# Kernel tuning notes

Hardware: AMD Instinct MI355X
Metric: run time of the kernel (lower is better)

The kernel has to match this reference:

```python
import jax, jax.numpy as jnp
import numpy as np

DIM = 1024
HEADS = 16
DIM_HEAD = 64
B = 4
N = 2048
INNER = HEADS * DIM_HEAD
SCALE = DIM_HEAD ** -0.5
NEG = -1e9


def setup_inputs() -> dict:
    key = jax.random.key(0)
    k1, k2, k3 = jax.random.split(key, 3)
    x = jax.random.normal(k1, (B, N, DIM), dtype=jnp.float32)
    w_qkv = jax.random.normal(k2, (DIM, 3 * INNER), dtype=jnp.float32) * (DIM ** -0.5)
    w_out = jax.random.normal(k3, (INNER, DIM), dtype=jnp.float32) * (INNER ** -0.5)
    b_out = jnp.zeros((DIM,), dtype=jnp.float32)
    return {"x": x, "w_qkv": w_qkv, "w_out": w_out, "b_out": b_out}


def reference(x, w_qkv, w_out, b_out):
    b, n, _ = x.shape
    qkv = x @ w_qkv  # [b, n, 3*inner]
    q, k, v = jnp.split(qkv, 3, axis=-1)
    # [b, n, inner] -> [b, h, n, d]
    split_heads = lambda t: t.reshape(b, n, HEADS, DIM_HEAD).transpose(0, 2, 1, 3)
    q, k, v = split_heads(q), split_heads(k), split_heads(v)
    dots = jnp.einsum('bhid,bhjd->bhij', q, k) * SCALE
    causal = jnp.tril(jnp.ones((n, n), dtype=bool))  # mask[i,j]=1 for j<=i
    dots = jnp.where(causal, dots, NEG)
    attn = jax.nn.softmax(dots, axis=-1)
    out = jnp.einsum('bhij,bhjd->bhid', attn, v)
    out = out.transpose(0, 2, 1, 3).reshape(b, n, INNER)
    return out @ w_out + b_out
```

## Files before the change

kernel.cpp:

```cpp
#include <hip/hip_runtime.h>

typedef unsigned short u16;
typedef __attribute__((ext_vector_type(8))) short short8;
typedef __attribute__((ext_vector_type(4))) float f32x4;
typedef __attribute__((ext_vector_type(4))) short short4v;

#define MFMA_BF16(a, b, c) __builtin_amdgcn_mfma_f32_16x16x32_bf16((a), (b), (c), 0, 0, 0)

__device__ __forceinline__ void gl2lds16(const u16* g, u16* l) {
  __builtin_amdgcn_global_load_lds(
      (const __attribute__((address_space(1))) unsigned int*)g,
      (__attribute__((address_space(3))) unsigned int*)l, 16, 0, 0);
}

__device__ __forceinline__ u16 f2bf(float f) {
  union { float f; unsigned u; } v; v.f = f;
  unsigned r = v.u + 0x7fffu + ((v.u >> 16) & 1u);
  return (u16)(r >> 16);
}

__global__ void fill_one_f32(float* p, int n) {
  int i = blockIdx.x * blockDim.x + threadIdx.x;
  if (i < n) p[i] = 1.0f;
}

__global__ void prep_k(const float* __restrict__ x, u16* __restrict__ Xb,
                       const float* __restrict__ w_qkv, u16* __restrict__ wqkvT,
                       const float* __restrict__ w_out, u16* __restrict__ woutT) {
  __shared__ float tile[32][33];
  const int bid = blockIdx.x, t = threadIdx.x;
  if (bid < 2048) {
    const int base = (bid * 256 + t) * 16;
#pragma unroll
    for (int h = 0; h < 2; ++h) {
      const f32x4 v0 = *(const f32x4*)&x[base + h * 8];
      const f32x4 v1 = *(const f32x4*)&x[base + h * 8 + 4];
      short8 o;
      o[0] = (short)f2bf(v0.x); o[1] = (short)f2bf(v0.y);
      o[2] = (short)f2bf(v0.z); o[3] = (short)f2bf(v0.w);
      o[4] = (short)f2bf(v1.x); o[5] = (short)f2bf(v1.y);
      o[6] = (short)f2bf(v1.z); o[7] = (short)f2bf(v1.w);
      *(short8*)&Xb[base + h * 8] = o;
    }
    return;
  }
  const float* src; u16* dst; int R, C, bx, by;
  if (bid < 5120) {
    const int tb = bid - 2048;
    src = w_qkv; dst = wqkvT; R = 1024; C = 3072; bx = tb % 96; by = tb / 96;
  } else {
    const int tb = bid - 5120;
    src = w_out; dst = woutT; R = 1024; C = 1024; bx = tb % 32; by = tb / 32;
  }
  const int tx = t & 31, ty = t >> 5;
  const int r0 = by * 32, c0 = bx * 32;
#pragma unroll
  for (int i = 0; i < 4; ++i)
    tile[ty + i * 8][tx] = src[(size_t)(r0 + ty + i * 8) * C + c0 + tx];
  __syncthreads();
#pragma unroll
  for (int i = 0; i < 4; ++i)
    dst[(size_t)(c0 + ty + i * 8) * R + r0 + tx] = f2bf(tile[tx][ty + i * 8]);
}

template <int MODE>
__launch_bounds__(256, 2)
__global__ void gemm_bt_k(const u16* __restrict__ A, const u16* __restrict__ Bt,
                          int K, int Ncols,
                          u16* __restrict__ O0, u16* __restrict__ O1,
                          u16* __restrict__ O2,
                          float* __restrict__ Of, const float* __restrict__ biasf) {
  __shared__ __align__(16) u16 Alds[128 * 32];
  __shared__ __align__(16) u16 Blds[128 * 32];
  const int t = threadIdx.x;
  const int w = t >> 6, l = t & 63;
  const int quad = l >> 4, l16 = l & 15;
  const int m0 = blockIdx.y * 128, n0 = blockIdx.x * 128;
  const int wm = w & 1, wn = w >> 1;

  f32x4 acc[4][4];
#pragma unroll
  for (int a = 0; a < 4; ++a)
#pragma unroll
    for (int b = 0; b < 4; ++b) acc[a][b] = (f32x4){0.f, 0.f, 0.f, 0.f};

  const int c0 = w * 128 + l;

#pragma unroll 1
  for (int k0 = 0; k0 < K; k0 += 32) {
    {
      int c = c0;
      gl2lds16(A + (size_t)(m0 + (c >> 2)) * K + k0 + (c & 3) * 8,
               (u16*)((char*)Alds + c * 16));
      gl2lds16(Bt + (size_t)(n0 + (c >> 2)) * K + k0 + (c & 3) * 8,
               (u16*)((char*)Blds + c * 16));
      c = c0 + 64;
      gl2lds16(A + (size_t)(m0 + (c >> 2)) * K + k0 + (c & 3) * 8,
               (u16*)((char*)Alds + c * 16));
      gl2lds16(Bt + (size_t)(n0 + (c >> 2)) * K + k0 + (c & 3) * 8,
               (u16*)((char*)Blds + c * 16));
    }
    __syncthreads();
    short8 av[4], bv[4];
#pragma unroll
    for (int a = 0; a < 4; ++a)
      av[a] = *(const short8*)&Alds[(wm * 64 + a * 16 + l16) * 32 + quad * 8];
#pragma unroll
    for (int b = 0; b < 4; ++b)
      bv[b] = *(const short8*)&Blds[(wn * 64 + b * 16 + l16) * 32 + quad * 8];
#pragma unroll
    for (int a = 0; a < 4; ++a)
#pragma unroll
      for (int b = 0; b < 4; ++b)
        acc[a][b] = MFMA_BF16(av[a], bv[b], acc[a][b]);
    __syncthreads();
  }

#pragma unroll
  for (int a = 0; a < 4; ++a)
#pragma unroll
    for (int b = 0; b < 4; ++b)
#pragma unroll
      for (int r = 0; r < 4; ++r) {
        const int row = m0 + wm * 64 + a * 16 + quad * 4 + r;
        const int col = n0 + wn * 64 + b * 16 + l16;
        const float v = acc[a][b][r];
        if (MODE == 0) {
          const int bb = row >> 11, n = row & 2047;
          const int which = col >> 10, j = col & 1023, h = j >> 6, d = j & 63;
          u16* dst = (which == 0) ? O0 : (which == 1) ? O1 : O2;
          dst[(((size_t)bb * 16 + h) * 2048 + n) * 64 + d] = f2bf(v);
        } else {
          Of[(size_t)row * Ncols + col] = v + biasf[col];
        }
      }
}

#define KS 72
__launch_bounds__(512, 4)
__global__ void flash_k4(const u16* __restrict__ Q, const u16* __restrict__ K,
                         const u16* __restrict__ V, u16* __restrict__ AO) {
  __shared__ __align__(16) u16 Klds[64 * KS];
  __shared__ __align__(16) u16 Vt[64 * KS];
  __shared__ __align__(16) u16 Plds[8][16 * KS];
  const int t = threadIdx.x, w = t >> 6, l = t & 63;
  const int quad = l >> 4, l16 = l & 15;
  const int bh = blockIdx.y;
  const size_t base = (size_t)bh * 2048 * 64;
  const u16* Qp = Q + base;
  const u16* Kp = K + base;
  const u16* Vp = V + base;
  const int bb = bh >> 4, hh = bh & 15;
  const float SC = 0.125f;
  const float FM = 3.0f;

  short8 ones;
#pragma unroll
  for (int j = 0; j < 8; ++j) ones[j] = (short)0x3F80;

#pragma unroll 1
  for (int ph = 0; ph < 2; ++ph) {
    const int qi = ph ? (15 - blockIdx.x) : blockIdx.x;
    const int qbase = qi * 128;

    const int qrow = qbase + w * 16 + l16;
    short8 qf[2];
    qf[0] = *(const short8*)&Qp[(size_t)qrow * 64 + quad * 8];
    qf[1] = *(const short8*)&Qp[(size_t)qrow * 64 + 32 + quad * 8];

    f32x4 oacc[4], lacc;
    lacc = (f32x4){0.f, 0.f, 0.f, 0.f};
#pragma unroll
    for (int df = 0; df < 4; ++df) oacc[df] = (f32x4){0.f, 0.f, 0.f, 0.f};

    const int nkt = 2 * qi + 2;
    const int wrow_lo = qbase + w * 16;
    const int wrow_hi = wrow_lo + 15;

#pragma unroll 1
    for (int kt = 0; kt < nkt; ++kt) {
      {
        const int kp = t >> 3, d0 = (t & 7) * 8;
        const short8 kv = *(const short8*)&Kp[(size_t)(kt * 64 + kp) * 64 + d0];
        const short8 vv = *(const short8*)&Vp[(size_t)(kt * 64 + kp) * 64 + d0];
        *(short8*)&Klds[kp * KS + d0] = kv;
#pragma unroll
        for (int j = 0; j < 8; ++j) Vt[(d0 + j) * KS + (kp ^ d0)] = (u16)vv[j];
      }
      __syncthreads();

      const bool skip = (kt * 64 > wrow_hi);
      if (!skip) {
        f32x4 sa[4];
#pragma unroll
        for (int nf = 0; nf < 4; ++nf) {
          const short8 kf0 = *(const short8*)&Klds[(nf * 16 + l16) * KS + quad * 8];
          const short8 kf1 = *(const short8*)&Klds[(nf * 16 + l16) * KS + 32 + quad * 8];
          f32x4 s = (f32x4){0.f, 0.f, 0.f, 0.f};
          s = MFMA_BF16(qf[0], kf0, s);
          s = MFMA_BF16(qf[1], kf1, s);
          sa[nf] = s;
        }

        const bool needmask = (kt * 64 + 63 > wrow_lo);
#pragma unroll
        for (int nf = 0; nf < 4; ++nf)
#pragma unroll
          for (int r = 0; r < 4; ++r) {
            float arg = fmaf(sa[nf][r], SC, -FM);
            if (needmask) {
              const int col = kt * 64 + nf * 16 + l16;
              const int row = qbase + w * 16 + quad * 4 + r;
              arg = (col <= row) ? arg : -1e9f;
            }
            union { float f; unsigned u; } pu;
            pu.f = __expf(arg);
            Plds[w][(quad * 4 + r) * KS + nf * 16 + l16] =
                (u16)((pu.u + 0x8000u) >> 16);
          }

        short8 pf[2];
        pf[0] = *(const short8*)&Plds[w][l16 * KS + quad * 8];
        pf[1] = *(const short8*)&Plds[w][l16 * KS + 32 + quad * 8];
        lacc = MFMA_BF16(pf[0], ones, lacc);
        lacc = MFMA_BF16(pf[1], ones, lacc);
#pragma unroll
        for (int df = 0; df < 4; ++df) {
          const int s = (2 * df + (l16 >> 3)) & 7;
          const int rowb = (df * 16 + l16) * KS;
          const short8 vf0 = *(const short8*)&Vt[rowb + ((quad ^ s) * 8)];
          const short8 vf1 = *(const short8*)&Vt[rowb + (((quad + 4) ^ s) * 8)];
          oacc[df] = MFMA_BF16(pf[0], vf0, oacc[df]);
          oacc[df] = MFMA_BF16(pf[1], vf1, oacc[df]);
        }
      }
      __syncthreads();
    }

    const int srow = qbase + w * 16 + quad * 4;
#pragma unroll
    for (int df = 0; df < 4; ++df)
#pragma unroll
      for (int r = 0; r < 4; ++r) {
        const int n = srow + r;
        const int d = df * 16 + l16;
        AO[((size_t)bb * 2048 + n) * 1024 + hh * 64 + d] =
            f2bf(oacc[df][r] / lacc[r]);
      }
  }
}

extern "C" void kernel_launch(void* const* d_in, const int* in_sizes, int n_in,
                              void* d_out, int out_size, void* d_ws, size_t ws_size,
                              hipStream_t stream) {
  const float* x = (const float*)d_in[0];
  const float* w_qkv = (const float*)d_in[1];
  const float* w_out = (const float*)d_in[2];
  const float* b_out = (const float*)d_in[3];
  float* out = (float*)d_out;

  const size_t MB = 1024 * 1024;
  if (ws_size < 72 * MB) {
    fill_one_f32<<<(out_size + 255) / 256, 256, 0, stream>>>(out, out_size);
    return;
  }

  char* ws = (char*)d_ws;
  u16* wqkvT = (u16*)(ws);
  u16* woutT = (u16*)(ws + 6 * MB);
  u16* Xb = (u16*)(ws + 8 * MB);
  u16* AO = Xb;
  u16* Qb = (u16*)(ws + 24 * MB);
  u16* Kb = (u16*)(ws + 40 * MB);
  u16* Vb = (u16*)(ws + 56 * MB);

  prep_k<<<6144, 256, 0, stream>>>(x, Xb, w_qkv, wqkvT, w_out, woutT);
  gemm_bt_k<0><<<dim3(3072 / 128, 8192 / 128), 256, 0, stream>>>(
      Xb, wqkvT, 1024, 3072, Qb, Kb, Vb, nullptr, nullptr);
  flash_k4<<<dim3(8, 64), 512, 0, stream>>>(Qb, Kb, Vb, AO);
  gemm_bt_k<1><<<dim3(1024 / 128, 8192 / 128), 256, 0, stream>>>(
      AO, woutT, 1024, 1024, nullptr, nullptr, nullptr, out, b_out);
}
```

Measured before the change: 265.4 us.

## Double-buffer K/V tiles in flash attention and pre-transpose V globally

Adds a separate kernel that transposes V into a [d, n] layout, so the flash kernel can store V tiles into LDS as whole vectors instead of scattering one element at a time. The flash kernel now double-buffers its K/V LDS tiles and prefetches the next tile into registers while computing the current one, which removes one barrier per iteration. It also remaps the grid to a flat 1D launch so that adjacent blocks cover different heads. The trade-offs are an extra kernel launch, an extra pass over V in global memory, more LDS per block, and 16 MB more workspace.

Measured after the change: 261.7 us. About the same (-1.4%).

```diff
diff --git a/kernel.cpp b/kernel.cpp
--- a/kernel.cpp
+++ b/kernel.cpp
@@ -3,7 +3,6 @@
 typedef unsigned short u16;
 typedef __attribute__((ext_vector_type(8))) short short8;
 typedef __attribute__((ext_vector_type(4))) float f32x4;
-typedef __attribute__((ext_vector_type(4))) short short4v;
 
 #define MFMA_BF16(a, b, c) __builtin_amdgcn_mfma_f32_16x16x32_bf16((a), (b), (c), 0, 0, 0)
 
@@ -61,6 +60,30 @@
 #pragma unroll
   for (int i = 0; i < 4; ++i)
     dst[(size_t)(c0 + ty + i * 8) * R + r0 + tx] = f2bf(tile[tx][ty + i * 8]);
+}
+
+__global__ void transpose_v(const u16* __restrict__ Vb, u16* __restrict__ VbT) {
+  __shared__ u16 tile[64 * 72];
+  const int t = threadIdx.x;
+  const int n0 = blockIdx.x * 64;
+  const size_t base = (size_t)blockIdx.y * 2048 * 64;
+#pragma unroll
+  for (int h = 0; h < 2; ++h) {
+    const int c = t + h * 256;
+    const int kp = c >> 3, d0 = (c & 7) * 8;
+    *(short8*)&tile[kp * 72 + d0] =
+        *(const short8*)&Vb[base + (size_t)(n0 + kp) * 64 + d0];
+  }
+  __syncthreads();
+#pragma unroll
+  for (int h = 0; h < 2; ++h) {
+    const int c = t + h * 256;
+    const int d = c >> 3, j0 = (c & 7) * 8;
+    short8 o;
+#pragma unroll
+    for (int i = 0; i < 8; ++i) o[i] = (short)tile[(j0 + i) * 72 + d];
+    *(short8*)&VbT[base + (size_t)d * 2048 + n0 + j0] = o;
+  }
 }
 
 template <int MODE>
@@ -138,29 +161,33 @@
 
 #define KS 72
 __launch_bounds__(512, 4)
-__global__ void flash_k4(const u16* __restrict__ Q, const u16* __restrict__ K,
-                         const u16* __restrict__ V, u16* __restrict__ AO) {
-  __shared__ __align__(16) u16 Klds[64 * KS];
-  __shared__ __align__(16) u16 Vt[64 * KS];
+__global__ void flash_k5(const u16* __restrict__ Q, const u16* __restrict__ K,
+                         const u16* __restrict__ VT, u16* __restrict__ AO) {
+  __shared__ __align__(16) u16 Klds[2][64 * KS];
+  __shared__ __align__(16) u16 Vt[2][64 * KS];
   __shared__ __align__(16) u16 Plds[8][16 * KS];
   const int t = threadIdx.x, w = t >> 6, l = t & 63;
   const int quad = l >> 4, l16 = l & 15;
-  const int bh = blockIdx.y;
+  const int flat = blockIdx.x;
+  const int qx = flat >> 6, bh = flat & 63;
   const size_t base = (size_t)bh * 2048 * 64;
   const u16* Qp = Q + base;
   const u16* Kp = K + base;
-  const u16* Vp = V + base;
+  const u16* VTp = VT + base;
   const int bb = bh >> 4, hh = bh & 15;
   const float SC = 0.125f;
   const float FM = 3.0f;
 
+  const int kcp = t >> 3, kcd = (t & 7) * 8;
+  const int vcd = t >> 3, vcp = (t & 7) * 8;
+
   short8 ones;
 #pragma unroll
   for (int j = 0; j < 8; ++j) ones[j] = (short)0x3F80;
 
 #pragma unroll 1
   for (int ph = 0; ph < 2; ++ph) {
-    const int qi = ph ? (15 - blockIdx.x) : blockIdx.x;
+    const int qi = ph ? (15 - qx) : qx;
     const int qbase = qi * 128;
 
     const int qrow = qbase + w * 16 + l16;
@@ -177,25 +204,28 @@
     const int wrow_lo = qbase + w * 16;
     const int wrow_hi = wrow_lo + 15;
 
+    short8 kv = *(const short8*)&Kp[(size_t)kcp * 64 + kcd];
+    short8 vv = *(const short8*)&VTp[(size_t)vcd * 2048 + vcp];
+
 #pragma unroll 1
     for (int kt = 0; kt < nkt; ++kt) {
-      {
-        const int kp = t >> 3, d0 = (t & 7) * 8;
-        const short8 kv = *(const short8*)&Kp[(size_t)(kt * 64 + kp) * 64 + d0];
-        const short8 vv = *(const short8*)&Vp[(size_t)(kt * 64 + kp) * 64 + d0];
-        *(short8*)&Klds[kp * KS + d0] = kv;
-#pragma unroll
-        for (int j = 0; j < 8; ++j) Vt[(d0 + j) * KS + (kp ^ d0)] = (u16)vv[j];
+      const int buf = kt & 1;
+      *(short8*)&Klds[buf][kcp * KS + kcd] = kv;
+      *(short8*)&Vt[buf][vcd * KS + vcp] = vv;
+      __syncthreads();
+
+      if (kt + 1 < nkt) {
+        kv = *(const short8*)&Kp[(size_t)((kt + 1) * 64 + kcp) * 64 + kcd];
+        vv = *(const short8*)&VTp[(size_t)vcd * 2048 + (kt + 1) * 64 + vcp];
       }
-      __syncthreads();
 
       const bool skip = (kt * 64 > wrow_hi);
       if (!skip) {
         f32x4 sa[4];
 #pragma unroll
         for (int nf = 0; nf < 4; ++nf) {
-          const short8 kf0 = *(const short8*)&Klds[(nf * 16 + l16) * KS + quad * 8];
-          const short8 kf1 = *(const short8*)&Klds[(nf * 16 + l16) * KS + 32 + quad * 8];
+          const short8 kf0 = *(const short8*)&Klds[buf][(nf * 16 + l16) * KS + quad * 8];
+          const short8 kf1 = *(const short8*)&Klds[buf][(nf * 16 + l16) * KS + 32 + quad * 8];
           f32x4 s = (f32x4){0.f, 0.f, 0.f, 0.f};
           s = MFMA_BF16(qf[0], kf0, s);
           s = MFMA_BF16(qf[1], kf1, s);
@@ -226,15 +256,13 @@
         lacc = MFMA_BF16(pf[1], ones, lacc);
 #pragma unroll
         for (int df = 0; df < 4; ++df) {
-          const int s = (2 * df + (l16 >> 3)) & 7;
           const int rowb = (df * 16 + l16) * KS;
-          const short8 vf0 = *(const short8*)&Vt[rowb + ((quad ^ s) * 8)];
-          const short8 vf1 = *(const short8*)&Vt[rowb + (((quad + 4) ^ s) * 8)];
+          const short8 vf0 = *(const short8*)&Vt[buf][rowb + quad * 8];
+          const short8 vf1 = *(const short8*)&Vt[buf][rowb + 32 + quad * 8];
           oacc[df] = MFMA_BF16(pf[0], vf0, oacc[df]);
           oacc[df] = MFMA_BF16(pf[1], vf1, oacc[df]);
         }
       }
-      __syncthreads();
     }
 
     const int srow = qbase + w * 16 + quad * 4;
@@ -247,6 +275,7 @@
         AO[((size_t)bb * 2048 + n) * 1024 + hh * 64 + d] =
             f2bf(oacc[df][r] / lacc[r]);
       }
+    __syncthreads();
   }
 }
 
@@ -260,7 +289,7 @@
   float* out = (float*)d_out;
 
   const size_t MB = 1024 * 1024;
-  if (ws_size < 72 * MB) {
+  if (ws_size < 88 * MB) {
     fill_one_f32<<<(out_size + 255) / 256, 256, 0, stream>>>(out, out_size);
     return;
   }
@@ -273,11 +302,13 @@
   u16* Qb = (u16*)(ws + 24 * MB);
   u16* Kb = (u16*)(ws + 40 * MB);
   u16* Vb = (u16*)(ws + 56 * MB);
+  u16* VbT = (u16*)(ws + 72 * MB);
 
   prep_k<<<6144, 256, 0, stream>>>(x, Xb, w_qkv, wqkvT, w_out, woutT);
   gemm_bt_k<0><<<dim3(3072 / 128, 8192 / 128), 256, 0, stream>>>(
       Xb, wqkvT, 1024, 3072, Qb, Kb, Vb, nullptr, nullptr);
-  flash_k4<<<dim3(8, 64), 512, 0, stream>>>(Qb, Kb, Vb, AO);
+  transpose_v<<<dim3(32, 64), 256, 0, stream>>>(Vb, VbT);
+  flash_k5<<<512, 512, 0, stream>>>(Qb, Kb, VbT, AO);
   gemm_bt_k<1><<<dim3(1024 / 128, 8192 / 128), 256, 0, stream>>>(
       AO, woutT, 1024, 1024, nullptr, nullptr, nullptr, out, b_out);
 }
```
